# Kernel tuning notes

Measured on AMD Instinct MI355X. Metric: run time of the kernel, lower is better.

The kernel has to match this reference:

```python
import jax, jax.numpy as jnp
import numpy as np

T, B, H = 512, 256, 512


def setup_inputs() -> dict:
    key = jax.random.key(0)
    k1, k2, k3, k4, k5 = jax.random.split(key, 5)
    scale_i = 1.0 / np.sqrt(H)
    return {
        "h0": jax.random.normal(k1, (B, H), dtype=jnp.float32),
        "ins": jax.random.normal(k2, (T, B, H), dtype=jnp.float32),
        "Wi": jax.random.normal(k3, (H, 3 * H), dtype=jnp.float32) * scale_i,
        "bi": jnp.zeros((3 * H,), dtype=jnp.float32),
        "Wh": jax.random.normal(k4, (H, 3 * H), dtype=jnp.float32) * scale_i,
        "bhn": jnp.zeros((H,), dtype=jnp.float32),
        "resets": jax.random.randint(k5, (T, B), 0, 2).astype(jnp.bool_),
    }


def reference(h0, ins, Wi, bi, Wh, bhn, resets):
    # flax GRUCell math: r = sig(x Wir + bir + h Whr); z = sig(x Wiz + biz + h Whz)
    def step(h, xr):
        x, reset = xr                       # x: [B,H], reset: [B]
        h = jnp.where(reset[:, None], jnp.zeros_like(h), h)  # reset carry to zeros
        gi = x @ Wi + bi                    # [B,3H]
        gh = h @ Wh                         # [B,3H]
        ir, iz, inn = jnp.split(gi, 3, axis=-1)
        hr, hz, hn = jnp.split(gh, 3, axis=-1)
        r = jax.nn.sigmoid(ir + hr)
        z = jax.nn.sigmoid(iz + hz)
        n = jnp.tanh(inn + r * (hn + bhn))
        h_new = (1.0 - z) * n + z * h
        return h_new, h_new

    _, ys = jax.lax.scan(step, h0, (ins, resets))
    return ys                               # [T,B,H]
```

## Files before the change

kernel.cpp:

```cpp
#include <hip/hip_runtime.h>
#include <hip/hip_cooperative_groups.h>

#define T_ 512
#define B_ 256
#define H_ 512
#define NBINS 4112
typedef __bf16 bf16_t;
typedef __bf16 bf16x8 __attribute__((ext_vector_type(8)));
typedef float f32x4 __attribute__((ext_vector_type(4)));

__device__ __forceinline__ float bf2f(unsigned short u) {
  unsigned x = ((unsigned)u) << 16; float f; __builtin_memcpy(&f, &x, 4); return f;
}
__device__ __forceinline__ bf16x8 pack2(f32x4 a, f32x4 b) {
  bf16x8 w;
#pragma unroll
  for (int i = 0; i < 4; ++i) { w[i] = (bf16_t)a[i]; w[i + 4] = (bf16_t)b[i]; }
  return w;
}
__device__ __forceinline__ void st_sc1(float* p, float v) {
  asm volatile("global_store_dword %0, %1, off sc0 sc1" :: "v"(p), "v"(v) : "memory");
}
__device__ __forceinline__ void ld8_sc1(const float* p0, const float* p1,
                                        const float* p2, const float* p3,
                                        const float* p4, const float* p5,
                                        const float* p6, const float* p7,
                                        f32x4& v0, f32x4& v1, f32x4& v2, f32x4& v3,
                                        f32x4& v4, f32x4& v5, f32x4& v6, f32x4& v7) {
  asm volatile(
      "global_load_dwordx4 %0, %8, off sc0 sc1\n\t"
      "global_load_dwordx4 %1, %9, off sc0 sc1\n\t"
      "global_load_dwordx4 %2, %10, off sc0 sc1\n\t"
      "global_load_dwordx4 %3, %11, off sc0 sc1\n\t"
      "global_load_dwordx4 %4, %12, off sc0 sc1\n\t"
      "global_load_dwordx4 %5, %13, off sc0 sc1\n\t"
      "global_load_dwordx4 %6, %14, off sc0 sc1\n\t"
      "global_load_dwordx4 %7, %15, off sc0 sc1\n\t"
      "s_waitcnt vmcnt(0)"
      : "=&v"(v0), "=&v"(v1), "=&v"(v2), "=&v"(v3),
        "=&v"(v4), "=&v"(v5), "=&v"(v6), "=&v"(v7)
      : "v"(p0), "v"(p1), "v"(p2), "v"(p3), "v"(p4), "v"(p5), "v"(p6), "v"(p7)
      : "memory");
}
__device__ __forceinline__ float sigm(float x) { return 1.f / (1.f + __expf(-x)); }
__device__ __forceinline__ float tanh_(float a) { return 1.f - 2.f / (__expf(2.f * a) + 1.f); }

__global__ __launch_bounds__(512) void zero_meta(int* __restrict__ flags,
                                                 int* __restrict__ bar) {
  int i = threadIdx.x;
  if (i < 4) flags[i] = 0;
  if (i < 8) bar[i] = 0;
}

__global__ __launch_bounds__(256) void detect_resets(const void* __restrict__ rst,
                                                     int n, int* __restrict__ flags) {
  const int* pi = (const int*)rst;
  const float* pf = (const float*)rst;
  int a = 0, bq = 0, c = 0;
  int nq = n >> 2;
  for (int i = blockIdx.x * 256 + threadIdx.x; i < nq; i += gridDim.x * 256) {
    int v = pi[i];
    if (v != 0 && v != 1) a = 1;
    float f = pf[i];
    if (!(f == 0.0f || f == 1.0f)) bq = 1;
    if ((i & 1) && v != 0) c = 1;
  }
  if (a) atomicOr(&flags[0], 1);
  if (bq) atomicOr(&flags[1], 1);
  if (c) atomicOr(&flags[2], 1);
}

__global__ __launch_bounds__(256) void convert_resets(const void* __restrict__ rst,
                                                      const int* __restrict__ flags,
                                                      unsigned char* __restrict__ r8,
                                                      int n) {
  const int* pi = (const int*)rst;
  const float* pf = (const float*)rst;
  int mode;
  if (flags[0] == 0) mode = flags[2] ? 0 : 3;
  else if (flags[1] == 0) mode = 1;
  else mode = 2;
  for (int i = blockIdx.x * 256 + threadIdx.x; i < n; i += gridDim.x * 256) {
    unsigned char v;
    if (mode == 0)      v = (unsigned char)(pi[i] != 0);
    else if (mode == 3) v = (unsigned char)(pi[2 * i] != 0);
    else if (mode == 1) v = (unsigned char)(pf[i] != 0.0f);
    else                v = ((const unsigned char*)rst)[i] ? 1 : 0;
    r8[i] = v;
  }
}

__global__ __launch_bounds__(256) void build_wc(const float* __restrict__ Wi,
                                                const float* __restrict__ Wh,
                                                bf16_t* __restrict__ Wc) {
  int id = blockIdx.x * 256 + threadIdx.x;
  int koct = id / 1536, n = id % 1536;
  const float* src = (koct < 64) ? Wi : Wh;
  int kk = (koct & 63) * 8;
  bf16x8 w;
#pragma unroll
  for (int e = 0; e < 8; ++e) w[e] = (bf16_t)src[(size_t)(kk + e) * 1536 + n];
  *(bf16x8*)(Wc + (size_t)id * 8) = w;
}

__device__ __forceinline__ int bucket_of(int t, int rs, int& p) {
  p = (t == 0 || rs) ? 0 : p + 1;
  return (p > 0) ? (p + 1) : ((t == 0 && !rs) ? 1 : 0);
}

__global__ __launch_bounds__(256) void phase_count(const unsigned char* __restrict__ r8,
                                                   int* __restrict__ fineCnt) {
  __shared__ int cl[NBINS];
  for (int i = threadIdx.x; i < NBINS; i += 256) cl[i] = 0;
  __syncthreads();
  int b = threadIdx.x, base = (b >> 5) * 514, p = 0;
  for (int t = 0; t < T_; ++t) {
    int bk = bucket_of(t, r8[t * B_ + b], p);
    atomicAdd(&cl[base + bk], 1);
  }
  __syncthreads();
  for (int i = threadIdx.x; i < NBINS; i += 256) fineCnt[i] = cl[i];
}

__global__ __launch_bounds__(1024) void scan_bins(const int* __restrict__ fineCnt,
                                                  int* __restrict__ cur) {
  __shared__ int s0[8192];
  __shared__ int s1[8192];
  int tid = threadIdx.x;
  for (int i = tid; i < 8192; i += 1024) s0[i] = (i < NBINS) ? fineCnt[i] : 0;
  __syncthreads();
  int* a = s0;
  int* bb = s1;
  for (int d = 1; d < 8192; d <<= 1) {
    for (int i = tid; i < 8192; i += 1024) bb[i] = a[i] + ((i >= d) ? a[i - d] : 0);
    __syncthreads();
    int* t = a; a = bb; bb = t;
  }
  for (int i = tid; i <= NBINS; i += 1024) cur[i] = (i == 0) ? 0 : a[i - 1];
}

__global__ __launch_bounds__(256) void scatter_elems(const unsigned char* __restrict__ r8,
                                                     const int* __restrict__ cur,
                                                     unsigned int* __restrict__ elem) {
  __shared__ int cl[NBINS];
  for (int i = threadIdx.x; i < NBINS; i += 256) cl[i] = cur[i];
  __syncthreads();
  int b = threadIdx.x, base = (b >> 5) * 514, p = 0;
  for (int t = 0; t < T_; ++t) {
    int bk = bucket_of(t, r8[t * B_ + b], p);
    int pos = atomicAdd(&cl[base + bk], 1);
    elem[pos] = (unsigned)(t * B_ + b);
  }
}

template <int NKS, int NRGC, int LDB>
__device__ __forceinline__ void mm_block(const char* lds, const char* W, int q,
                                         int rgb, int span, int nrgd, int am, int aq,
                                         f32x4 (&acc)[4][NRGC]) {
  const char* Bp = W + (size_t)(q * 16 + am) * 16;
#pragma unroll
  for (int ks = 0; ks < NKS; ++ks) {
    const int koct = ks * 4 + aq;
    const char* bb = Bp + (size_t)koct * 24576;
    bf16x8 b0 = *(const bf16x8*)(bb);
    bf16x8 b1 = *(const bf16x8*)(bb + 8192);
    bf16x8 b2 = *(const bf16x8*)(bb + 16384);
#pragma unroll
    for (int rg = 0; rg < NRGC; ++rg) {
      if (rg >= rgb && rg < rgb + span && rg < nrgd) {
        const int ar = rg * 16 + am;
        bf16x8 af = *(const bf16x8*)(lds + (size_t)ar * LDB +
                                     ((koct * 16) ^ ((ar & 7) << 4)));
        acc[0][rg] = __builtin_amdgcn_mfma_f32_16x16x32_bf16(af, b0, acc[0][rg], 0, 0, 0);
        acc[1][rg] = __builtin_amdgcn_mfma_f32_16x16x32_bf16(af, b1, acc[1][rg], 0, 0, 0);
        if (ks < 16)
          acc[2][rg] = __builtin_amdgcn_mfma_f32_16x16x32_bf16(af, b2, acc[2][rg], 0, 0, 0);
        else
          acc[3][rg] = __builtin_amdgcn_mfma_f32_16x16x32_bf16(af, b2, acc[3][rg], 0, 0, 0);
      }
    }
  }
}

__global__ __launch_bounds__(512, 2) void bucket0_gemm(
    const float* __restrict__ ins, const bf16_t* __restrict__ Wc,
    const float* __restrict__ bi, const float* __restrict__ bhn,
    const unsigned int* __restrict__ elem, const int* __restrict__ cur,
    float* __restrict__ out) {
  extern __shared__ char lds[];
  const int g = blockIdx.y, u = blockIdx.x;
  const int beg = cur[g * 514];
  const int cnt = cur[g * 514 + 1] - beg;
  if (u * 128 >= cnt) return;
  const int tid = threadIdx.x, lane = tid & 63, w = tid >> 6;
  const int am = lane & 15, aq = lane >> 4;
  {
    const int tr = tid >> 2, tl = tid & 3;
    const int row = u * 128 + tr;
    const float* hs = (row < cnt) ? (ins + (size_t)elem[beg + row] * 512) : nullptr;
    const int swz = (tr & 7) << 4;
#pragma unroll 4
    for (int cc = 0; cc < 16; ++cc) {
      int koct = tl + 4 * cc;
      bf16x8 wv;
      if (hs) {
        f32x4 a0 = *(const f32x4*)(hs + koct * 8);
        f32x4 a1 = *(const f32x4*)(hs + koct * 8 + 4);
        wv = pack2(a0, a1);
      } else {
#pragma unroll
        for (int z = 0; z < 8; ++z) wv[z] = (bf16_t)0.f;
      }
      *(bf16x8*)(lds + tr * 1024 + ((koct * 16) ^ swz)) = wv;
    }
  }
  __syncthreads();
  const int rem = cnt - u * 128;
  const int nrgd = ((rem < 128 ? rem : 128) + 15) >> 4;
#pragma unroll 1
  for (int s = 0; s < 4; ++s) {
    const int q = w + 8 * s;
    f32x4 acc[4][8];
#pragma unroll
    for (int gg = 0; gg < 4; ++gg)
#pragma unroll
      for (int r = 0; r < 8; ++r) acc[gg][r] = (f32x4){0.f, 0.f, 0.f, 0.f};
    mm_block<16, 8, 1024>(lds, (const char*)Wc, q, 0, 8, nrgd, am, aq, acc);
    const int j = q * 16 + am;
    const float bir = bi[j], biz = bi[512 + j], bin = bi[1024 + j], bh = bhn[j];
#pragma unroll
    for (int rg = 0; rg < 8; ++rg) {
      if (rg < nrgd) {
#pragma unroll
        for (int qq = 0; qq < 4; ++qq) {
          const int row = u * 128 + rg * 16 + aq * 4 + qq;
          if (row < cnt) {
            float r = sigm(acc[0][rg][qq] + bir);
            float z = sigm(acc[1][rg][qq] + biz);
            float n = tanh_(acc[2][rg][qq] + bin + r * bh);
            st_sc1(out + (size_t)elem[beg + row] * 512 + j, (1.f - z) * n);
          }
        }
      }
    }
  }
}

__global__ __launch_bounds__(512, 2) void gru_phases(
    const float* __restrict__ ins, const float* __restrict__ h0,
    const bf16_t* __restrict__ Wc, const float* __restrict__ bi,
    const float* __restrict__ bhn, const unsigned int* __restrict__ elem,
    const int* __restrict__ cur, int* __restrict__ bar, float* __restrict__ out) {
  extern __shared__ char lds[];
  const int tid = threadIdx.x, lane = tid & 63, w = tid >> 6;
  const int am = lane & 15, aq = lane >> 4;
  const int g = blockIdx.x >> 5, bg = blockIdx.x & 31;
  const int base = g * 514;

  for (int it = 0; it <= 512; ++it) {
    const int beg = cur[base + it + 1];
    const int cnt = cur[base + it + 2] - beg;
    if (it >= 1 && cnt == 0) break;
    if (cnt > 0) {
      const int ntiles = (cnt + 63) >> 6;
      int lg = 0;
      while (lg < 4 && (ntiles << lg) < 32) ++lg;
      const int nitems = ntiles << lg;
      const int Q = 32 >> lg;
      for (int i = bg; i < nitems; i += 32) {
        const int u = i >> lg, jc = i & ((1 << lg) - 1);
        __syncthreads();
        {
          const int tr = tid >> 3, tl = tid & 7;
          const int row = u * 64 + tr;
          const float* xs = nullptr;
          const float* ph = nullptr;
          if (row < cnt) {
            const unsigned e = elem[beg + row];
            xs = ins + (size_t)e * 512;
            ph = (e < 256) ? (h0 + (size_t)e * 512) : (out + ((size_t)e - 256) * 512);
          }
          const int swz = (tr & 7) << 4;
#pragma unroll 1
          for (int bt = 0; bt < 4; ++bt) {
            const float* srcb = (bt < 2) ? xs : ph;
            f32x4 v[8];
            if (xs) {
              const float* p[8];
#pragma unroll
              for (int s2 = 0; s2 < 4; ++s2) {
                int ko = tl + 8 * (bt * 4 + s2);
                p[2 * s2] = srcb + (ko & 63) * 8;
                p[2 * s2 + 1] = srcb + (ko & 63) * 8 + 4;
              }
              ld8_sc1(p[0], p[1], p[2], p[3], p[4], p[5], p[6], p[7],
                      v[0], v[1], v[2], v[3], v[4], v[5], v[6], v[7]);
            } else {
#pragma unroll
              for (int z = 0; z < 8; ++z) v[z] = (f32x4){0.f, 0.f, 0.f, 0.f};
            }
#pragma unroll
            for (int s2 = 0; s2 < 4; ++s2) {
              int koct = tl + 8 * (bt * 4 + s2);
              *(bf16x8*)(lds + tr * 2048 + ((koct * 16) ^ swz)) =
                  pack2(v[2 * s2], v[2 * s2 + 1]);
            }
          }
        }
        __syncthreads();
        const int rem = cnt - u * 64;
        const int nrgd = ((rem < 64 ? rem : 64) + 15) >> 4;
        const int span = (Q >= 8) ? 4 : (Q >> 1);
        const int rgb = (Q >= 8) ? 0 : (w / Q) * span;
        const int nq = (Q >= 8) ? (Q >> 3) : 1;
#pragma unroll 1
        for (int s = 0; s < nq; ++s) {
          const int q = (Q >= 8) ? (jc * Q + w + 8 * s) : (jc * Q + (w & (Q - 1)));
          f32x4 acc[4][4];
#pragma unroll
          for (int gg = 0; gg < 4; ++gg)
#pragma unroll
            for (int r = 0; r < 4; ++r) acc[gg][r] = (f32x4){0.f, 0.f, 0.f, 0.f};
          mm_block<32, 4, 2048>(lds, (const char*)Wc, q, rgb, span, nrgd, am, aq, acc);
          const int j = q * 16 + am;
          const float bir = bi[j], biz = bi[512 + j], bin = bi[1024 + j], bh = bhn[j];
#pragma unroll
          for (int rg = 0; rg < 4; ++rg) {
            if (rg >= rgb && rg < rgb + span && rg < nrgd) {
#pragma unroll
              for (int qq = 0; qq < 4; ++qq) {
                const int lrow = rg * 16 + aq * 4 + qq;
                const int row = u * 64 + lrow;
                if (row < cnt) {
                  const unsigned e = elem[beg + row];
                  unsigned short hraw = *(const unsigned short*)(
                      lds + (size_t)lrow * 2048 +
                      (((64 + (j >> 3)) * 16) ^ ((lrow & 7) << 4)) + (j & 7) * 2);
                  float hp = bf2f(hraw);
                  float r = sigm(acc[0][rg][qq] + bir);
                  float z = sigm(acc[1][rg][qq] + biz);
                  float n = tanh_(acc[2][rg][qq] + bin + r * (acc[3][rg][qq] + bh));
                  st_sc1(out + (size_t)e * 512 + j, (1.f - z) * n + z * hp);
                }
              }
            }
          }
        }
      }
    }
    __syncthreads();
    if (tid == 0) {
      __hip_atomic_fetch_add(&bar[g], 1, __ATOMIC_RELAXED, __HIP_MEMORY_SCOPE_AGENT);
      const int target = 32 * (it + 1);
      while (__hip_atomic_load(&bar[g], __ATOMIC_RELAXED, __HIP_MEMORY_SCOPE_AGENT) <
             target) {
        __builtin_amdgcn_s_sleep(8);
      }
    }
    __syncthreads();
  }
}

extern "C" void kernel_launch(void* const* d_in, const int* in_sizes, int n_in,
                              void* d_out, int out_size, void* d_ws, size_t ws_size,
                              hipStream_t stream) {
  const float* h0  = (const float*)d_in[0];
  const float* ins = (const float*)d_in[1];
  const float* Wi  = (const float*)d_in[2];
  const float* bi  = (const float*)d_in[3];
  const float* Wh  = (const float*)d_in[4];
  const float* bhn = (const float*)d_in[5];
  const void*  rst = d_in[6];
  float* out = (float*)d_out;

  char* ws = (char*)d_ws;
  const size_t off_r8    = 0;
  const size_t off_Wc    = 131072;
  const size_t off_flags = 3276800;
  const size_t off_bar   = 3276864;
  const size_t off_fcnt  = 3276928;
  const size_t off_cur   = 3293440;
  const size_t off_elem  = 3309952;
  const size_t need      = 3834240;
  if (ws_size < need) return;

  unsigned char* r8 = (unsigned char*)(ws + off_r8);
  bf16_t* Wc = (bf16_t*)(ws + off_Wc);
  int* flags = (int*)(ws + off_flags);
  int* bar = (int*)(ws + off_bar);
  int* fineCnt = (int*)(ws + off_fcnt);
  int* cur = (int*)(ws + off_cur);
  unsigned int* elem = (unsigned int*)(ws + off_elem);

  zero_meta<<<1, 512, 0, stream>>>(flags, bar);
  detect_resets<<<64, 256, 0, stream>>>(rst, T_ * B_, flags);
  convert_resets<<<128, 256, 0, stream>>>(rst, flags, r8, T_ * B_);
  build_wc<<<768, 256, 0, stream>>>(Wi, Wh, Wc);
  phase_count<<<1, 256, 0, stream>>>(r8, fineCnt);
  scan_bins<<<1, 1024, 0, stream>>>(fineCnt, cur);
  scatter_elems<<<1, 256, 0, stream>>>(r8, cur, elem);

  (void)hipFuncSetAttribute((const void*)bucket0_gemm,
                            hipFuncAttributeMaxDynamicSharedMemorySize, 131072);
  (void)hipFuncSetAttribute((const void*)gru_phases,
                            hipFuncAttributeMaxDynamicSharedMemorySize, 131072);

  bucket0_gemm<<<dim3(128, 8), 512, 131072, stream>>>(ins, Wc, bi, bhn, elem, cur, out);

  void* args[] = {(void*)&ins, (void*)&h0, (void*)&Wc, (void*)&bi, (void*)&bhn,
                  (void*)&elem, (void*)&cur, (void*)&bar, (void*)&out};
  (void)hipLaunchCooperativeKernel((const void*)gru_phases, dim3(256), dim3(512),
                                   args, 131072, stream);
}
```

Measured before the change: 1.338 ms.

## Fuse binning kernels and fold bucket-0 GEMM into persistent GRU kernel

Merges the three single-block binning kernels (count, scan, scatter) into one kernel, and moves the standalone bucket-0 GEMM into the cooperative persistent kernel as iteration zero. The aim is to cut kernel launches and inter-kernel gaps. The x-operand staging now uses nontemporal loads and is separated from the coherent sc1 loads of h. The spin-wait sleep is also shortened. The risk is that bucket-0 work is spread over only 32 blocks per group instead of a wide separate grid, and it now sits inside the serial barrier chain.

```diff
diff --git a/kernel.cpp b/kernel.cpp
--- a/kernel.cpp
+++ b/kernel.cpp
@@ -1,5 +1,4 @@
 #include <hip/hip_runtime.h>
-#include <hip/hip_cooperative_groups.h>
 
 #define T_ 512
 #define B_ 256
@@ -45,8 +44,8 @@
 __device__ __forceinline__ float sigm(float x) { return 1.f / (1.f + __expf(-x)); }
 __device__ __forceinline__ float tanh_(float a) { return 1.f - 2.f / (__expf(2.f * a) + 1.f); }
 
-__global__ __launch_bounds__(512) void zero_meta(int* __restrict__ flags,
-                                                 int* __restrict__ bar) {
+__global__ __launch_bounds__(64) void zero_meta(int* __restrict__ flags,
+                                                int* __restrict__ bar) {
   int i = threadIdx.x;
   if (i < 4) flags[i] = 0;
   if (i < 8) bar[i] = 0;
@@ -108,26 +107,22 @@
   return (p > 0) ? (p + 1) : ((t == 0 && !rs) ? 1 : 0);
 }
 
-__global__ __launch_bounds__(256) void phase_count(const unsigned char* __restrict__ r8,
-                                                   int* __restrict__ fineCnt) {
-  __shared__ int cl[NBINS];
-  for (int i = threadIdx.x; i < NBINS; i += 256) cl[i] = 0;
+__global__ __launch_bounds__(1024) void bins_kernel(const unsigned char* __restrict__ r8,
+                                                    int* __restrict__ cur,
+                                                    unsigned int* __restrict__ elem) {
+  extern __shared__ int sm[];
+  int* s0 = sm;
+  int* s1 = sm + 8192;
+  const int tid = threadIdx.x;
+  for (int i = tid; i < 8192; i += 1024) s0[i] = 0;
   __syncthreads();
-  int b = threadIdx.x, base = (b >> 5) * 514, p = 0;
-  for (int t = 0; t < T_; ++t) {
-    int bk = bucket_of(t, r8[t * B_ + b], p);
-    atomicAdd(&cl[base + bk], 1);
-  }
-  __syncthreads();
-  for (int i = threadIdx.x; i < NBINS; i += 256) fineCnt[i] = cl[i];
-}
-
-__global__ __launch_bounds__(1024) void scan_bins(const int* __restrict__ fineCnt,
-                                                  int* __restrict__ cur) {
-  __shared__ int s0[8192];
-  __shared__ int s1[8192];
-  int tid = threadIdx.x;
-  for (int i = tid; i < 8192; i += 1024) s0[i] = (i < NBINS) ? fineCnt[i] : 0;
+  if (tid < 256) {
+    int b = tid, base = (b >> 5) * 514, p = 0;
+    for (int t = 0; t < T_; ++t) {
+      int bk = bucket_of(t, r8[t * B_ + b], p);
+      atomicAdd(&s0[base + bk], 1);
+    }
+  }
   __syncthreads();
   int* a = s0;
   int* bb = s1;
@@ -137,19 +132,16 @@
     int* t = a; a = bb; bb = t;
   }
   for (int i = tid; i <= NBINS; i += 1024) cur[i] = (i == 0) ? 0 : a[i - 1];
-}
-
-__global__ __launch_bounds__(256) void scatter_elems(const unsigned char* __restrict__ r8,
-                                                     const int* __restrict__ cur,
-                                                     unsigned int* __restrict__ elem) {
-  __shared__ int cl[NBINS];
-  for (int i = threadIdx.x; i < NBINS; i += 256) cl[i] = cur[i];
+  for (int i = tid; i < 8192; i += 1024)
+    bb[i] = (i == 0) ? 0 : ((i <= NBINS) ? a[i - 1] : 0);
   __syncthreads();
-  int b = threadIdx.x, base = (b >> 5) * 514, p = 0;
-  for (int t = 0; t < T_; ++t) {
-    int bk = bucket_of(t, r8[t * B_ + b], p);
-    int pos = atomicAdd(&cl[base + bk], 1);
-    elem[pos] = (unsigned)(t * B_ + b);
+  if (tid < 256) {
+    int b = tid, base = (b >> 5) * 514, p = 0;
+    for (int t = 0; t < T_; ++t) {
+      int bk = bucket_of(t, r8[t * B_ + b], p);
+      int pos = atomicAdd(&bb[base + bk], 1);
+      elem[pos] = (unsigned)(t * B_ + b);
+    }
   }
 }
 
@@ -182,70 +174,6 @@
   }
 }
 
-__global__ __launch_bounds__(512, 2) void bucket0_gemm(
-    const float* __restrict__ ins, const bf16_t* __restrict__ Wc,
-    const float* __restrict__ bi, const float* __restrict__ bhn,
-    const unsigned int* __restrict__ elem, const int* __restrict__ cur,
-    float* __restrict__ out) {
-  extern __shared__ char lds[];
-  const int g = blockIdx.y, u = blockIdx.x;
-  const int beg = cur[g * 514];
-  const int cnt = cur[g * 514 + 1] - beg;
-  if (u * 128 >= cnt) return;
-  const int tid = threadIdx.x, lane = tid & 63, w = tid >> 6;
-  const int am = lane & 15, aq = lane >> 4;
-  {
-    const int tr = tid >> 2, tl = tid & 3;
-    const int row = u * 128 + tr;
-    const float* hs = (row < cnt) ? (ins + (size_t)elem[beg + row] * 512) : nullptr;
-    const int swz = (tr & 7) << 4;
-#pragma unroll 4
-    for (int cc = 0; cc < 16; ++cc) {
-      int koct = tl + 4 * cc;
-      bf16x8 wv;
-      if (hs) {
-        f32x4 a0 = *(const f32x4*)(hs + koct * 8);
-        f32x4 a1 = *(const f32x4*)(hs + koct * 8 + 4);
-        wv = pack2(a0, a1);
-      } else {
-#pragma unroll
-        for (int z = 0; z < 8; ++z) wv[z] = (bf16_t)0.f;
-      }
-      *(bf16x8*)(lds + tr * 1024 + ((koct * 16) ^ swz)) = wv;
-    }
-  }
-  __syncthreads();
-  const int rem = cnt - u * 128;
-  const int nrgd = ((rem < 128 ? rem : 128) + 15) >> 4;
-#pragma unroll 1
-  for (int s = 0; s < 4; ++s) {
-    const int q = w + 8 * s;
-    f32x4 acc[4][8];
-#pragma unroll
-    for (int gg = 0; gg < 4; ++gg)
-#pragma unroll
-      for (int r = 0; r < 8; ++r) acc[gg][r] = (f32x4){0.f, 0.f, 0.f, 0.f};
-    mm_block<16, 8, 1024>(lds, (const char*)Wc, q, 0, 8, nrgd, am, aq, acc);
-    const int j = q * 16 + am;
-    const float bir = bi[j], biz = bi[512 + j], bin = bi[1024 + j], bh = bhn[j];
-#pragma unroll
-    for (int rg = 0; rg < 8; ++rg) {
-      if (rg < nrgd) {
-#pragma unroll
-        for (int qq = 0; qq < 4; ++qq) {
-          const int row = u * 128 + rg * 16 + aq * 4 + qq;
-          if (row < cnt) {
-            float r = sigm(acc[0][rg][qq] + bir);
-            float z = sigm(acc[1][rg][qq] + biz);
-            float n = tanh_(acc[2][rg][qq] + bin + r * bh);
-            st_sc1(out + (size_t)elem[beg + row] * 512 + j, (1.f - z) * n);
-          }
-        }
-      }
-    }
-  }
-}
-
 __global__ __launch_bounds__(512, 2) void gru_phases(
     const float* __restrict__ ins, const float* __restrict__ h0,
     const bf16_t* __restrict__ Wc, const float* __restrict__ bi,
@@ -257,11 +185,67 @@
   const int g = blockIdx.x >> 5, bg = blockIdx.x & 31;
   const int base = g * 514;
 
-  for (int it = 0; it <= 512; ++it) {
-    const int beg = cur[base + it + 1];
-    const int cnt = cur[base + it + 2] - beg;
-    if (it >= 1 && cnt == 0) break;
-    if (cnt > 0) {
+  for (int it = 0; it <= 513; ++it) {
+    const int beg = cur[base + it];
+    const int cnt = cur[base + it + 1] - beg;
+    if (it >= 2 && cnt == 0) break;
+    if (cnt > 0 && it == 0) {
+      const int ntiles = (cnt + 127) >> 7;
+      for (int u = bg; u < ntiles; u += 32) {
+        __syncthreads();
+        {
+          const int tr = tid >> 2, tl = tid & 3;
+          const int row = u * 128 + tr;
+          const float* xs = (row < cnt) ? (ins + (size_t)elem[beg + row] * 512) : nullptr;
+          const int swz = (tr & 7) << 4;
+          char* lrp = lds + tr * 1024;
+#pragma unroll 4
+          for (int s2 = 0; s2 < 16; ++s2) {
+            const int ko = tl + 4 * s2;
+            bf16x8 wv;
+            if (xs) {
+              f32x4 a0 = __builtin_nontemporal_load((const f32x4*)(xs + ko * 8));
+              f32x4 a1 = __builtin_nontemporal_load((const f32x4*)(xs + ko * 8 + 4));
+              wv = pack2(a0, a1);
+            } else {
+#pragma unroll
+              for (int z = 0; z < 8; ++z) wv[z] = (bf16_t)0.f;
+            }
+            *(bf16x8*)(lrp + ((ko * 16) ^ swz)) = wv;
+          }
+        }
+        __syncthreads();
+        const int rem = cnt - u * 128;
+        const int nrgd = ((rem < 128 ? rem : 128) + 15) >> 4;
+#pragma unroll 1
+        for (int s = 0; s < 4; ++s) {
+          const int q = w + 8 * s;
+          f32x4 acc[4][8];
+#pragma unroll
+          for (int gg = 0; gg < 4; ++gg)
+#pragma unroll
+            for (int r = 0; r < 8; ++r) acc[gg][r] = (f32x4){0.f, 0.f, 0.f, 0.f};
+          mm_block<16, 8, 1024>(lds, (const char*)Wc, q, 0, 8, nrgd, am, aq, acc);
+          const int j = q * 16 + am;
+          const float bir = bi[j], biz = bi[512 + j], bin = bi[1024 + j], bh = bhn[j];
+#pragma unroll
+          for (int rg = 0; rg < 8; ++rg) {
+            if (rg < nrgd) {
+#pragma unroll
+              for (int qq = 0; qq < 4; ++qq) {
+                const int row = u * 128 + rg * 16 + aq * 4 + qq;
+                if (row < cnt) {
+                  float r = sigm(acc[0][rg][qq] + bir);
+                  float z = sigm(acc[1][rg][qq] + biz);
+                  float n = tanh_(acc[2][rg][qq] + bin + r * bh);
+                  st_sc1(out + (size_t)elem[beg + row] * 512 + j, (1.f - z) * n);
+                }
+              }
+            }
+          }
+        }
+      }
+    } else if (cnt > 0) {
       const int ntiles = (cnt + 63) >> 6;
       int lg = 0;
       while (lg < 4 && (ntiles << lg) < 32) ++lg;
@@ -281,29 +265,48 @@
             ph = (e < 256) ? (h0 + (size_t)e * 512) : (out + ((size_t)e - 256) * 512);
           }
           const int swz = (tr & 7) << 4;
+          char* lrp = lds + tr * 2048;
+#pragma unroll
+          for (int s2 = 0; s2 < 8; ++s2) {
+            const int ko = tl + 8 * s2;
+            bf16x8 wv;
+            if (xs) {
+              f32x4 a0 = __builtin_nontemporal_load((const f32x4*)(xs + ko * 8));
+              f32x4 a1 = __builtin_nontemporal_load((const f32x4*)(xs + ko * 8 + 4));
+              wv = pack2(a0, a1);
+            } else {
+#pragma unroll
+              for (int z = 0; z < 8; ++z) wv[z] = (bf16_t)0.f;
+            }
+            *(bf16x8*)(lrp + ((ko * 16) ^ swz)) = wv;
+          }
+          if (ph) {
 #pragma unroll 1
-          for (int bt = 0; bt < 4; ++bt) {
-            const float* srcb = (bt < 2) ? xs : ph;
-            f32x4 v[8];
-            if (xs) {
-              const float* p[8];
+            for (int hb = 0; hb < 2; ++hb) {
+              f32x4 hv[8];
+              const float* hp[8];
 #pragma unroll
               for (int s2 = 0; s2 < 4; ++s2) {
-                int ko = tl + 8 * (bt * 4 + s2);
-                p[2 * s2] = srcb + (ko & 63) * 8;
-                p[2 * s2 + 1] = srcb + (ko & 63) * 8 + 4;
+                const int ko = tl + 8 * (8 + hb * 4 + s2);
+                hp[2 * s2] = ph + (ko & 63) * 8;
+                hp[2 * s2 + 1] = ph + (ko & 63) * 8 + 4;
               }
-              ld8_sc1(p[0], p[1], p[2], p[3], p[4], p[5], p[6], p[7],
-                      v[0], v[1], v[2], v[3], v[4], v[5], v[6], v[7]);
-            } else {
-#pragma unroll
-              for (int z = 0; z < 8; ++z) v[z] = (f32x4){0.f, 0.f, 0.f, 0.f};
-            }
-#pragma unroll
-            for (int s2 = 0; s2 < 4; ++s2) {
-              int koct = tl + 8 * (bt * 4 + s2);
-              *(bf16x8*)(lds + tr * 2048 + ((koct * 16) ^ swz)) =
-                  pack2(v[2 * s2], v[2 * s2 + 1]);
+              ld8_sc1(hp[0], hp[1], hp[2], hp[3], hp[4], hp[5], hp[6], hp[7],
+                      hv[0], hv[1], hv[2], hv[3], hv[4], hv[5], hv[6], hv[7]);
+#pragma unroll
+              for (int s2 = 0; s2 < 4; ++s2) {
+                const int ko = tl + 8 * (8 + hb * 4 + s2);
+                *(bf16x8*)(lrp + ((ko * 16) ^ swz)) = pack2(hv[2 * s2], hv[2 * s2 + 1]);
+              }
+            }
+          } else {
+#pragma unroll
+            for (int s2 = 0; s2 < 8; ++s2) {
+              const int ko = tl + 8 * (8 + s2);
+              bf16x8 wv;
+#pragma unroll
+              for (int z = 0; z < 8; ++z) wv[z] = (bf16_t)0.f;
+              *(bf16x8*)(lrp + ((ko * 16) ^ swz)) = wv;
             }
           }
         }
@@ -354,7 +357,7 @@
       const int target = 32 * (it + 1);
       while (__hip_atomic_load(&bar[g], __ATOMIC_RELAXED, __HIP_MEMORY_SCOPE_AGENT) <
              target) {
-        __builtin_amdgcn_s_sleep(8);
+        __builtin_amdgcn_s_sleep(2);
       }
     }
     __syncthreads();
@@ -378,35 +381,28 @@
   const size_t off_Wc    = 131072;
   const size_t off_flags = 3276800;
   const size_t off_bar   = 3276864;
-  const size_t off_fcnt  = 3276928;
-  const size_t off_cur   = 3293440;
-  const size_t off_elem  = 3309952;
-  const size_t need      = 3834240;
+  const size_t off_cur   = 3276928;
+  const size_t off_elem  = 3293440;
+  const size_t need      = 3817728;
   if (ws_size < need) return;
 
   unsigned char* r8 = (unsigned char*)(ws + off_r8);
   bf16_t* Wc = (bf16_t*)(ws + off_Wc);
   int* flags = (int*)(ws + off_flags);
   int* bar = (int*)(ws + off_bar);
-  int* fineCnt = (int*)(ws + off_fcnt);
   int* cur = (int*)(ws + off_cur);
   unsigned int* elem = (unsigned int*)(ws + off_elem);
 
-  zero_meta<<<1, 512, 0, stream>>>(flags, bar);
+  zero_meta<<<1, 64, 0, stream>>>(flags, bar);
   detect_resets<<<64, 256, 0, stream>>>(rst, T_ * B_, flags);
   convert_resets<<<128, 256, 0, stream>>>(rst, flags, r8, T_ * B_);
   build_wc<<<768, 256, 0, stream>>>(Wi, Wh, Wc);
-  phase_count<<<1, 256, 0, stream>>>(r8, fineCnt);
-  scan_bins<<<1, 1024, 0, stream>>>(fineCnt, cur);
-  scatter_elems<<<1, 256, 0, stream>>>(r8, cur, elem);
-
-  (void)hipFuncSetAttribute((const void*)bucket0_gemm,
-                            hipFuncAttributeMaxDynamicSharedMemorySize, 131072);
+  (void)hipFuncSetAttribute((const void*)bins_kernel,
+                            hipFuncAttributeMaxDynamicSharedMemorySize, 65536);
+  bins_kernel<<<1, 1024, 65536, stream>>>(r8, cur, elem);
+
   (void)hipFuncSetAttribute((const void*)gru_phases,
                             hipFuncAttributeMaxDynamicSharedMemorySize, 131072);
-
-  bucket0_gemm<<<dim3(128, 8), 512, 131072, stream>>>(ins, Wc, bi, bhn, elem, cur, out);
-
   void* args[] = {(void*)&ins, (void*)&h0, (void*)&Wc, (void*)&bi, (void*)&bhn,
                   (void*)&elem, (void*)&cur, (void*)&bar, (void*)&out};
   (void)hipLaunchCooperativeKernel((const void*)gru_phases, dim3(256), dim3(512),
```

Result: slower. 1.484 ms (+10.9%).
